# Kernel optimization log

Hardware: AMD Instinct MI355X
Metric: run time of the kernel (lower is better)

The kernel has to match this reference:

```python
import jax, jax.numpy as jnp
import numpy as np

B, C, D, H, W = 2, 512, 32, 32, 32
L, CTX = 256, 768
NH, HD, G = 8, 64, 8
EPS = 1e-5


def group_norm(x, w, b):
    Bb, Cc, Dd, Hh, Ww = x.shape
    xg = x.reshape(Bb, G, Cc // G, Dd, Hh, Ww)
    mu = xg.mean(axis=(2, 3, 4, 5), keepdims=True)
    var = xg.var(axis=(2, 3, 4, 5), keepdims=True)
    xn = ((xg - mu) * jax.lax.rsqrt(var + EPS)).reshape(Bb, Cc, Dd, Hh, Ww)
    return xn * w[None, :, None, None, None] + b[None, :, None, None, None]


def layer_norm(x, w, b):
    mu = x.mean(axis=-1, keepdims=True)
    var = x.var(axis=-1, keepdims=True)
    return (x - mu) * jax.lax.rsqrt(var + EPS) * w + b


def setup_inputs() -> dict:
    key = jax.random.key(0)
    ks = jax.random.split(key, 8)
    s = 0.02  # weight init scale
    return {
        "x": jax.random.normal(ks[0], (B, C, D, H, W), jnp.float32),
        "context": jax.random.normal(ks[1], (B, L, CTX), jnp.float32),
        "gn_w": jnp.ones((C,), jnp.float32),
        "gn_b": jnp.zeros((C,), jnp.float32),
        "ln_w": jnp.ones((CTX,), jnp.float32),
        "ln_b": jnp.zeros((CTX,), jnp.float32),
        "q_w": jax.random.normal(ks[2], (C, C), jnp.float32) * s,
        "q_b": jnp.zeros((C,), jnp.float32),
        "k_w": jax.random.normal(ks[3], (C, CTX), jnp.float32) * s,
        "k_b": jnp.zeros((C,), jnp.float32),
        "v_w": jax.random.normal(ks[4], (C, CTX), jnp.float32) * s,
        "v_b": jnp.zeros((C,), jnp.float32),
        "proj_w": jax.random.normal(ks[5], (C, C), jnp.float32) * s,
        "proj_b": jnp.zeros((C,), jnp.float32),
    }


def reference(x, context, gn_w, gn_b, ln_w, ln_b, q_w, q_b, k_w, k_b, v_w, v_b, proj_w, proj_b):
    Bb, Cc, Dd, Hh, Ww = x.shape
    S = Dd * Hh * Ww
    h = group_norm(x, gn_w, gn_b)
    ctx = layer_norm(context, ln_w, ln_b)
    # 1x1 Conv3d == per-voxel linear over channels
    q = jnp.einsum('oc,bcdhw->bodhw', q_w, h) + q_b[None, :, None, None, None]
    q = q.reshape(Bb, NH, HD, S)                                        # (b,h,e,s)
    k = (ctx @ k_w.T + k_b).reshape(Bb, L, NH, HD).transpose(0, 2, 1, 3)  # (b,h,l,e)
    v = (ctx @ v_w.T + v_b).reshape(Bb, L, NH, HD).transpose(0, 2, 1, 3)  # (b,h,l,e)
    scale = HD ** -0.5
    attn = jnp.einsum('bhes,bhle->bhsl', q, k) * scale                  # (b,h,S,L)
    attn = jax.nn.softmax(attn, axis=-1)
    out = jnp.einsum('bhsl,bhle->bhes', attn, v).reshape(Bb, Cc, Dd, Hh, Ww)
    out = jnp.einsum('oc,bcdhw->bodhw', proj_w, out) + proj_b[None, :, None, None, None]
    return out + x
```

## Files before the change

### kernel.cpp

```cpp
#include <hip/hip_runtime.h>

typedef unsigned short u16;
typedef unsigned int u32;
typedef __attribute__((ext_vector_type(4))) float f32x4;
typedef __attribute__((ext_vector_type(8))) short bf16x8;
typedef __attribute__((ext_vector_type(8))) u16 u16x8;
typedef __attribute__((ext_vector_type(4))) u16 u16x4;
typedef __attribute__((ext_vector_type(4))) u32 u32x4;

#define DEVI __device__ __forceinline__

constexpr int C_ = 512, S_ = 32768, L_ = 256, CTX_ = 768;

DEVI u16 f2b(float f) {
    union { float f; unsigned u; } x; x.f = f;
    unsigned r = x.u + 0x7fffu + ((x.u >> 16) & 1u);
    return (u16)(r >> 16);
}

DEVI f32x4 mfma16(bf16x8 a, bf16x8 b, f32x4 c) {
    return __builtin_amdgcn_mfma_f32_16x16x32_bf16(a, b, c, 0, 0, 0);
}

DEVI void gload16(const void* g, void* l) {
    __builtin_amdgcn_global_load_lds(
        (const __attribute__((address_space(1))) void*)g,
        (__attribute__((address_space(3))) void*)l, 16, 0, 0);
}

DEVI u32 cvtpk(float lo, float hi) {
    u32 d;
    asm("v_cvt_pk_bf16_f32 %0, %1, %2" : "=v"(d) : "v"(lo), "v"(hi));
    return d;
}
DEVI void pl32(u32& a, u32& b) {
    asm volatile("v_permlane32_swap_b32 %0, %1" : "+v"(a), "+v"(b));
}
DEVI void pl16(u32& a, u32& b) {
    asm volatile("v_permlane16_swap_b32 %0, %1" : "+v"(a), "+v"(b));
}

__global__ __launch_bounds__(256) void prep_small(
    const float* __restrict__ a0, const float* __restrict__ a1,
    const float* __restrict__ a2, const float* __restrict__ a3,
    u16* __restrict__ o0, u16* __restrict__ o1,
    u16* __restrict__ o2, u16* __restrict__ o3,
    const float* __restrict__ ctx, const float* __restrict__ lw,
    const float* __restrict__ lb, u16* __restrict__ cn)
{
    const int which = blockIdx.y, tid = threadIdx.x;
    if (which < 4) {
        const float* src = which == 0 ? a0 : which == 1 ? a1 : which == 2 ? a2 : a3;
        u16* dst = which == 0 ? o0 : which == 1 ? o1 : which == 2 ? o2 : o3;
        int n4 = (which == 1 || which == 2) ? (512 * 768 / 4) : (512 * 512 / 4);
        int i = blockIdx.x * 256 + tid;
        if (i < n4) {
            float4 v = ((const float4*)src)[i];
            u16x4 o; o[0] = f2b(v.x); o[1] = f2b(v.y); o[2] = f2b(v.z); o[3] = f2b(v.w);
            ((u16x4*)dst)[i] = o;
        }
        return;
    }
    const int row = blockIdx.x;
    const float* p = ctx + (size_t)row * CTX_;
    float v0 = p[tid], v1 = p[tid + 256], v2 = p[tid + 512];
    float s1 = v0 + v1 + v2, s2 = v0 * v0 + v1 * v1 + v2 * v2;
    for (int m = 1; m < 64; m <<= 1) { s1 += __shfl_xor(s1, m); s2 += __shfl_xor(s2, m); }
    __shared__ float a1s[4], a2s[4];
    int w = tid >> 6, lane = tid & 63;
    if (lane == 0) { a1s[w] = s1; a2s[w] = s2; }
    __syncthreads();
    s1 = a1s[0] + a1s[1] + a1s[2] + a1s[3];
    s2 = a2s[0] + a2s[1] + a2s[2] + a2s[3];
    const float invN = 1.0f / 768.0f;
    float mu = s1 * invN, rstd = rsqrtf(s2 * invN - mu * mu + 1e-5f);
    u16* o = cn + (size_t)row * CTX_;
    o[tid]       = f2b((v0 - mu) * rstd * lw[tid]       + lb[tid]);
    o[tid + 256] = f2b((v1 - mu) * rstd * lw[tid + 256] + lb[tid + 256]);
    o[tid + 512] = f2b((v2 - mu) * rstd * lw[tid + 512] + lb[tid + 512]);
}

__global__ __launch_bounds__(256) void gn_partial(const float* __restrict__ x,
                                                  float* __restrict__ part)
{
    const int bg = blockIdx.y, blk = blockIdx.x, tid = threadIdx.x;
    const int cs = blk >> 5, sblk = blk & 31;
    const float* base = x + (size_t)(bg * 64 + cs * 32) * S_
                          + (size_t)sblk * 1024 + tid * 4;
    float s1 = 0.f, s2 = 0.f;
    for (int c = 0; c < 32; ++c) {
        float4 v = *(const float4*)(base + (size_t)c * S_);
        s1 += v.x + v.y + v.z + v.w;
        s2 += v.x * v.x + v.y * v.y + v.z * v.z + v.w * v.w;
    }
    for (int m = 1; m < 64; m <<= 1) { s1 += __shfl_xor(s1, m); s2 += __shfl_xor(s2, m); }
    __shared__ float a1[4], a2[4];
    int w = tid >> 6, lane = tid & 63;
    if (lane == 0) { a1[w] = s1; a2[w] = s2; }
    __syncthreads();
    if (tid == 0) {
        part[(bg * 64 + blk) * 2 + 0] = a1[0] + a1[1] + a1[2] + a1[3];
        part[(bg * 64 + blk) * 2 + 1] = a2[0] + a2[1] + a2[2] + a2[3];
    }
}

__global__ __launch_bounds__(64) void gn_final_coef(
    const float* __restrict__ part, const float* __restrict__ gw,
    const float* __restrict__ gb, float* __restrict__ ca, float* __restrict__ cb)
{
    int bg = blockIdx.x, tid = threadIdx.x;
    float s1 = part[(bg * 64 + tid) * 2];
    float s2 = part[(bg * 64 + tid) * 2 + 1];
    for (int m = 1; m < 64; m <<= 1) { s1 += __shfl_xor(s1, m); s2 += __shfl_xor(s2, m); }
    const float invN = 1.0f / (64.0f * (float)S_);
    float mu = __shfl(s1, 0) * invN;
    float var = __shfl(s2, 0) * invN - mu * mu;
    float rs = rsqrtf(var + 1e-5f);
    int z = bg >> 3, c = (bg & 7) * 64 + tid;
    float a = rs * gw[c];
    ca[z * 512 + c] = a;
    cb[z * 512 + c] = gb[c] - mu * a;
}

template <int MODE, bool SWAP>
__global__ __launch_bounds__(256, 4) void gemm_nt(
    const u16* __restrict__ A, const u16* __restrict__ Bp,
    const float* __restrict__ bias, void* __restrict__ outp,
    const float* __restrict__ resid, int K, int ldo,
    size_t aStride, size_t bStride, size_t oStride, float scale,
    const u16* __restrict__ Bp2, const float* __restrict__ bias2,
    void* __restrict__ outp2)
{
    __shared__ __align__(16) u16 lA[2][4096];
    __shared__ __align__(16) u16 lB[2][4096];
    const int tid = threadIdx.x;
    const int w = tid >> 6, lane = tid & 63;
    const int g = lane >> 4, r = lane & 15;

    const int nx = gridDim.x, nxy = nx * gridDim.y;
    const int raw = blockIdx.x + nx * blockIdx.y;
    const int tile = (raw & 7) * (nxy >> 3) + (raw >> 3);
    const int bx = tile % nx, by = tile / nx;
    const int m0 = (SWAP ? by : bx) * 128, n0 = (SWAP ? bx : by) * 128;
    const int z = blockIdx.z;
    A += (size_t)z * aStride;
    const u16* Bsel = Bp;
    if constexpr (MODE == 3) { if (z) Bsel = Bp2; }
    Bsel += (size_t)z * bStride;

    const int l8 = lane & 7, lh = lane >> 3;
    const int u_ = l8 ^ lh;
    const int mro = (lh << 1) + (u_ >> 2);
    const int kco = (u_ & 3) * 8;
    const int wr = w >> 1, wc = w & 1;
    const int nt = K >> 5;

    f32x4 acc[4][4];
#pragma unroll
    for (int m = 0; m < 4; ++m)
#pragma unroll
        for (int n = 0; n < 4; ++n) acc[m][n] = f32x4{0.f, 0.f, 0.f, 0.f};

#define STAGE_B(t, bi_) {                                                      \
    size_t ko_ = (size_t)((t) * 32 + kco);                                     \
    _Pragma("unroll")                                                          \
    for (int j = 0; j < 2; ++j) {                                              \
        int grow_ = w * 32 + j * 16 + mro;                                     \
        gload16(Bsel + (size_t)(n0 + grow_) * K + ko_,                         \
                &lB[bi_][(w * 16 + j * 8) << 6]);                              \
    } }

#define STAGE_A(t, bi_) {                                                      \
    size_t ko_ = (size_t)((t) * 32 + kco);                                     \
    _Pragma("unroll")                                                          \
    for (int j = 0; j < 2; ++j) {                                              \
        int grow_ = w * 32 + j * 16 + mro;                                     \
        gload16(A + (size_t)(m0 + grow_) * K + ko_,                            \
                &lA[bi_][(w * 16 + j * 8) << 6]);                              \
    } }

    const float* xA = nullptr;
    const float* cAp = nullptr;
    const float* cBp = nullptr;
    int cp2 = 0, sb = 0, zc = 0;
    f32x4 a00{}, a01{}, a10{}, a11{};
    float2 ka{}, kb{};
    if constexpr (MODE == 4) {
        xA = resid + (size_t)z * ((size_t)C_ * S_);
        cAp = bias2;
        cBp = (const float*)outp2;
        cp2 = (tid >> 4) * 2;
        sb = (tid & 15) * 8;
        zc = z * 512;
    }

#define LOAD_A4(t) {                                                           \
    int c0n_ = (t) * 32 + cp2;                                                 \
    const float* r0_ = xA + (size_t)c0n_ * S_ + m0 + sb;                       \
    a00 = *(const f32x4*)r0_;  a01 = *(const f32x4*)(r0_ + 4);                 \
    a10 = *(const f32x4*)(r0_ + S_); a11 = *(const f32x4*)(r0_ + S_ + 4);      \
    ka = *(const float2*)&cAp[zc + c0n_];                                      \
    kb = *(const float2*)&cBp[zc + c0n_]; }

#define WRITE_A4(bi_) {                                                        \
    _Pragma("unroll")                                                          \
    for (int j = 0; j < 8; ++j) {                                              \
        float v0_ = ((j < 4) ? a00[j] : a01[j - 4]) * ka.x + kb.x;             \
        float v1_ = ((j < 4) ? a10[j] : a11[j - 4]) * ka.y + kb.y;             \
        int mm_ = sb + j;                                                      \
        int idx_ = ((mm_ >> 1) << 6)                                           \
            + (((((mm_ & 1) << 2) + (cp2 >> 3)) ^ ((mm_ >> 1) & 7)) << 3)      \
            + (cp2 & 7);                                                       \
        *(u32*)&lA[bi_][idx_] = cvtpk(v0_, v1_);                               \
    } }

    if constexpr (MODE == 4) {
        STAGE_B(0, 0);
        LOAD_A4(0);
        WRITE_A4(0);
        __syncthreads();
        for (int t = 0; t < nt; ++t) {
            const int cur = t & 1;
            if (t + 1 < nt) {
                STAGE_B(t + 1, cur ^ 1);
                LOAD_A4(t + 1);
            }
            bf16x8 af[4], bf_[4];
#pragma unroll
            for (int m = 0; m < 4; ++m) {
                int row = wr * 32 + m * 8 + (r >> 1);
                int slot = (((r & 1) << 2) + g) ^ ((r >> 1) & 7);
                af[m] = *(const bf16x8*)&lA[cur][(row << 6) + (slot << 3)];
            }
#pragma unroll
            for (int n = 0; n < 4; ++n) {
                int row = wc * 32 + n * 8 + (r >> 1);
                int slot = (((r & 1) << 2) + g) ^ ((r >> 1) & 7);
                bf_[n] = *(const bf16x8*)&lB[cur][(row << 6) + (slot << 3)];
            }
#pragma unroll
            for (int m = 0; m < 4; ++m)
#pragma unroll
                for (int n = 0; n < 4; ++n)
                    acc[m][n] = mfma16(bf_[n], af[m], acc[m][n]);
            if (t + 1 < nt) WRITE_A4(cur ^ 1);
            __syncthreads();
        }
    } else {
        STAGE_A(0, 0);
        STAGE_B(0, 0);
        for (int t = 0; t < nt; ++t) {
            const int cur = t & 1;
            if (t + 1 < nt) {
                STAGE_A(t + 1, cur ^ 1);
                STAGE_B(t + 1, cur ^ 1);
                asm volatile("s_waitcnt vmcnt(4)" ::: "memory");
            } else {
                asm volatile("s_waitcnt vmcnt(0)" ::: "memory");
            }
            __builtin_amdgcn_s_barrier();
            bf16x8 af[4], bf_[4];
#pragma unroll
            for (int m = 0; m < 4; ++m) {
                int row = wr * 32 + m * 8 + (r >> 1);
                int slot = (((r & 1) << 2) + g) ^ ((r >> 1) & 7);
                af[m] = *(const bf16x8*)&lA[cur][(row << 6) + (slot << 3)];
            }
#pragma unroll
            for (int n = 0; n < 4; ++n) {
                int row = wc * 32 + n * 8 + (r >> 1);
                int slot = (((r & 1) << 2) + g) ^ ((r >> 1) & 7);
                bf_[n] = *(const bf16x8*)&lB[cur][(row << 6) + (slot << 3)];
            }
#pragma unroll
            for (int m = 0; m < 4; ++m)
#pragma unroll
                for (int n = 0; n < 4; ++n)
                    acc[m][n] = mfma16(bf_[n], af[m], acc[m][n]);
            __builtin_amdgcn_s_barrier();
        }
    }
#undef STAGE_A
#undef STAGE_B
#undef LOAD_A4
#undef WRITE_A4

    if constexpr (MODE == 0 || MODE == 4) {
        u16* ob = (u16*)outp + (size_t)z * oStride;
#pragma unroll
        for (int m = 0; m < 4; ++m) {
            int gm = m0 + wr * 64 + m * 16 + r;
#pragma unroll
            for (int n = 0; n < 4; ++n) {
                int gn0 = n0 + wc * 64 + n * 16 + g * 4;
                float4 bn = *(const float4*)&bias[gn0];
                u32 w0 = cvtpk(acc[m][n][0] * scale + bn.x * scale,
                               acc[m][n][1] * scale + bn.y * scale);
                u32 w1 = cvtpk(acc[m][n][2] * scale + bn.z * scale,
                               acc[m][n][3] * scale + bn.w * scale);
                *(uint2*)&ob[(size_t)gm * ldo + gn0] = make_uint2(w0, w1);
            }
        }
    } else if constexpr (MODE == 2) {
        float* of = (float*)outp + (size_t)z * oStride;
        const float* rs = resid + (size_t)z * oStride;
#pragma unroll
        for (int m = 0; m < 4; ++m) {
            int gm = m0 + wr * 64 + m * 16 + r;
            float bm = bias[gm];
#pragma unroll
            for (int n = 0; n < 4; ++n) {
                int gn0 = n0 + wc * 64 + n * 16 + g * 4;
                size_t idx = (size_t)gm * ldo + gn0;
                float4 rv = *(const float4*)&rs[idx];
                float4 o4;
                o4.x = acc[m][n][0] + bm + rv.x;
                o4.y = acc[m][n][1] + bm + rv.y;
                o4.z = acc[m][n][2] + bm + rv.z;
                o4.w = acc[m][n][3] + bm + rv.w;
                *(float4*)&of[idx] = o4;
            }
        }
    } else if constexpr (MODE == 3) {
        if (z == 0) {
            u16* ob = (u16*)outp;
#pragma unroll
            for (int m = 0; m < 4; ++m) {
                int gm = m0 + wr * 64 + m * 16 + r;
#pragma unroll
                for (int n = 0; n < 4; ++n) {
                    int gn0 = n0 + wc * 64 + n * 16 + g * 4;
                    float4 bn = *(const float4*)&bias[gn0];
                    u32 w0 = cvtpk(acc[m][n][0] + bn.x, acc[m][n][1] + bn.y);
                    u32 w1 = cvtpk(acc[m][n][2] + bn.z, acc[m][n][3] + bn.w);
                    *(uint2*)&ob[(size_t)gm * ldo + gn0] = make_uint2(w0, w1);
                }
            }
        } else {
            u16* ob = (u16*)outp2;
#pragma unroll
            for (int m = 0; m < 4; ++m) {
                int gm = m0 + wr * 64 + m * 16 + r;
                int bb = gm >> 8, l = gm & 255;
#pragma unroll
                for (int n = 0; n < 4; ++n) {
                    int gn0 = n0 + wc * 64 + n * 16 + g * 4;
#pragma unroll
                    for (int i = 0; i < 4; ++i)
                        ob[((size_t)(bb * 512 + gn0 + i)) * 256 + l] =
                            f2b(acc[m][n][i] + bias2[gn0 + i]);
                }
            }
        }
    }
}

__global__ __launch_bounds__(256, 2) void attn_kernel(
    const u16* __restrict__ q, const u16* __restrict__ kk,
    const u16* __restrict__ vv, u16* __restrict__ ao)
{
    __shared__ __align__(16) u16 sm[32768];
    const int tid = threadIdx.x;
    const int w = tid >> 6, lane = tid & 63;
    const int g = lane >> 4, r = lane & 15;
    const int bh = blockIdx.y, b = bh >> 3, h = bh & 7;
    const int s0 = blockIdx.x * 128;

    {
        const u16* kbase = kk + ((size_t)b * L_) * C_ + h * 64;
#pragma unroll
        for (int j = 0; j < 8; ++j) {
            int idx = j * 256 + tid;
            int l = idx >> 3, ch = idx & 7;
            u16x8 val = *(const u16x8*)(kbase + (size_t)l * C_ + ch * 8);
            *(u16x8*)&sm[l * 64 + ((ch ^ (l & 7)) << 3)] = val;
        }
        const u16* vbase = vv + ((size_t)bh * 64) * 256;
#pragma unroll
        for (int j = 0; j < 8; ++j) {
            int idx = j * 256 + tid;
            int e = idx >> 5, ch = idx & 31;
            u16x8 val = *(const u16x8*)(vbase + (size_t)e * 256 + ch * 8);
            *(u16x8*)&sm[16384 + e * 256 + ((ch ^ (e & 7)) << 3)] = val;
        }
    }

    const int sw = s0 + w * 32;
    bf16x8 qf[2][2];
#pragma unroll
    for (int m = 0; m < 2; ++m)
#pragma unroll
        for (int kt = 0; kt < 2; ++kt)
            qf[m][kt] = *(const bf16x8*)(q + ((size_t)(b * S_ + sw + m * 16 + r)) * C_
                                         + h * 64 + kt * 32 + g * 8);
    __syncthreads();

    f32x4 accs[2][16];
#pragma unroll
    for (int m = 0; m < 2; ++m)
#pragma unroll
        for (int n = 0; n < 16; ++n) accs[m][n] = f32x4{0.f, 0.f, 0.f, 0.f};
    __builtin_amdgcn_s_setprio(1);
#pragma unroll
    for (int n = 0; n < 16; ++n) {
#pragma unroll
        for (int kt = 0; kt < 2; ++kt) {
            int c = kt * 4 + g;
            bf16x8 kf = *(const bf16x8*)&sm[(n * 16 + r) * 64 + ((c ^ (r & 7)) << 3)];
#pragma unroll
            for (int m = 0; m < 2; ++m) accs[m][n] = mfma16(kf, qf[m][kt], accs[m][n]);
        }
    }
    __builtin_amdgcn_s_setprio(0);

    float inv[2];
#pragma unroll
    for (int m = 0; m < 2; ++m) {
        float mx = accs[m][0][0];
#pragma unroll
        for (int n = 0; n < 16; ++n)
#pragma unroll
            for (int i = 0; i < 4; ++i) mx = fmaxf(mx, accs[m][n][i]);
        mx = fmaxf(mx, __shfl_xor(mx, 16));
        mx = fmaxf(mx, __shfl_xor(mx, 32));
        float sum = 0.f;
#pragma unroll
        for (int n = 0; n < 16; ++n)
#pragma unroll
            for (int i = 0; i < 4; ++i) {
                float e = __expf(accs[m][n][i] - mx);
                accs[m][n][i] = e; sum += e;
            }
        sum += __shfl_xor(sum, 16);
        sum += __shfl_xor(sum, 32);
        inv[m] = 1.0f / sum;
    }

    f32x4 acco[2][4];
#pragma unroll
    for (int m = 0; m < 2; ++m)
#pragma unroll
        for (int n = 0; n < 4; ++n) acco[m][n] = f32x4{0.f, 0.f, 0.f, 0.f};

#pragma unroll
    for (int c = 0; c < 8; ++c) {
        bf16x8 pa[2];
#pragma unroll
        for (int m = 0; m < 2; ++m) {
            u32 x0 = cvtpk(accs[m][2 * c][0] * inv[m], accs[m][2 * c][1] * inv[m]);
            u32 x1 = cvtpk(accs[m][2 * c][2] * inv[m], accs[m][2 * c][3] * inv[m]);
            u32 y0 = cvtpk(accs[m][2 * c + 1][0] * inv[m], accs[m][2 * c + 1][1] * inv[m]);
            u32 y1 = cvtpk(accs[m][2 * c + 1][2] * inv[m], accs[m][2 * c + 1][3] * inv[m]);
            pl32(x0, y0);
            pl32(x1, y1);
            pl16(x0, y0);
            pl16(x1, y1);
            u32x4 pw; pw[0] = x0; pw[1] = x1; pw[2] = y0; pw[3] = y1;
            pa[m] = *(bf16x8*)&pw;
        }
        bf16x8 vf[4];
#pragma unroll
        for (int n = 0; n < 4; ++n) {
            int e = n * 16 + r;
            vf[n] = *(const bf16x8*)&sm[16384 + e * 256 + (((c * 4 + g) ^ (r & 7)) << 3)];
        }
        __builtin_amdgcn_s_setprio(1);
#pragma unroll
        for (int m = 0; m < 2; ++m)
#pragma unroll
            for (int n = 0; n < 4; ++n)
                acco[m][n] = mfma16(vf[n], pa[m], acco[m][n]);
        __builtin_amdgcn_s_setprio(0);
    }

#pragma unroll
    for (int m = 0; m < 2; ++m) {
        const size_t rowb = ((size_t)(b * S_ + sw + m * 16 + r)) * C_ + h * 64;
#pragma unroll
        for (int n = 0; n < 4; ++n) {
            u32 w0 = cvtpk(acco[m][n][0], acco[m][n][1]);
            u32 w1 = cvtpk(acco[m][n][2], acco[m][n][3]);
            *(uint2*)&ao[rowb + n * 16 + g * 4] = make_uint2(w0, w1);
        }
    }
}

extern "C" void kernel_launch(void* const* d_in, const int* in_sizes, int n_in,
                              void* d_out, int out_size, void* d_ws, size_t ws_size,
                              hipStream_t stream)
{
    (void)in_sizes; (void)n_in; (void)out_size; (void)ws_size;
    const float* x    = (const float*)d_in[0];
    const float* ctx  = (const float*)d_in[1];
    const float* gn_w = (const float*)d_in[2];
    const float* gn_b = (const float*)d_in[3];
    const float* ln_w = (const float*)d_in[4];
    const float* ln_b = (const float*)d_in[5];
    const float* q_w  = (const float*)d_in[6];
    const float* q_b  = (const float*)d_in[7];
    const float* k_w  = (const float*)d_in[8];
    const float* k_b  = (const float*)d_in[9];
    const float* v_w  = (const float*)d_in[10];
    const float* v_b  = (const float*)d_in[11];
    const float* p_w  = (const float*)d_in[12];
    const float* p_b  = (const float*)d_in[13];
    float* out = (float*)d_out;

    char* ws = (char*)d_ws;
    constexpr size_t WS_WQ   = 0;
    constexpr size_t WS_WK   = WS_WQ + (size_t)512 * 512 * 2;
    constexpr size_t WS_WV   = WS_WK + (size_t)512 * 768 * 2;
    constexpr size_t WS_WP   = WS_WV + (size_t)512 * 768 * 2;
    constexpr size_t WS_PART = WS_WP + (size_t)512 * 512 * 2;
    constexpr size_t WS_CA   = WS_PART + (size_t)16 * 64 * 2 * 4;
    constexpr size_t WS_CB   = WS_CA + 4096;
    constexpr size_t WS_CTXN = WS_CB + 4096;
    constexpr size_t WS_K    = WS_CTXN + (size_t)512 * 768 * 2;
    constexpr size_t WS_V    = WS_K + (size_t)2 * 8 * 256 * 64 * 2;
    constexpr size_t WS_Q    = WS_V + (size_t)2 * 8 * 256 * 64 * 2;
    constexpr size_t WS_H    = WS_Q + (size_t)2 * 32768 * 512 * 2;

    u16* wq = (u16*)(ws + WS_WQ);
    u16* wk = (u16*)(ws + WS_WK);
    u16* wv = (u16*)(ws + WS_WV);
    u16* wp = (u16*)(ws + WS_WP);
    float* part  = (float*)(ws + WS_PART);
    float* coefA = (float*)(ws + WS_CA);
    float* coefB = (float*)(ws + WS_CB);
    u16* ctxn = (u16*)(ws + WS_CTXN);
    u16* kt   = (u16*)(ws + WS_K);
    u16* vt   = (u16*)(ws + WS_V);
    u16* qt   = (u16*)(ws + WS_Q);
    u16* ao   = (u16*)(ws + WS_H);

    const size_t bsc = (size_t)S_ * C_;

    gn_partial<<<dim3(64, 16), 256, 0, stream>>>(x, part);
    prep_small<<<dim3(512, 5), 256, 0, stream>>>(q_w, k_w, v_w, p_w,
                                                 wq, wk, wv, wp,
                                                 ctx, ln_w, ln_b, ctxn);
    gn_final_coef<<<16, 64, 0, stream>>>(part, gn_w, gn_b, coefA, coefB);
    gemm_nt<4, true><<<dim3(4, 256, 2), 256, 0, stream>>>(
        nullptr, wq, q_b, qt, x, 512, 512, 0, 0, bsc, 0.125f,
        nullptr, coefA, coefB);
    gemm_nt<3, false><<<dim3(4, 4, 2), 256, 0, stream>>>(
        ctxn, wk, k_b, kt, nullptr, 768, 512, 0, 0, 0, 1.0f,
        wv, v_b, vt);
    attn_kernel<<<dim3(256, 16), 256, 0, stream>>>(qt, kt, vt, ao);
    gemm_nt<2, false><<<dim3(4, 256, 2), 256, 0, stream>>>(
        wp, ao, p_b, out, x, 512, S_, 0, bsc, bsc, 1.0f,
        nullptr, nullptr, nullptr);
}
```

Baseline: 270.7 us.

## Fold GroupNorm affine into Q weights and feed bf16 x copy to Q GEMM

New measurement: 275.6 us. Within noise of the previous version (+1.8%).

```diff
diff --git a/kernel.cpp b/kernel.cpp
--- a/kernel.cpp
+++ b/kernel.cpp
@@ -81,17 +81,21 @@
 }
 
 __global__ __launch_bounds__(256) void gn_partial(const float* __restrict__ x,
-                                                  float* __restrict__ part)
+                                                  float* __restrict__ part,
+                                                  u16* __restrict__ xbf)
 {
     const int bg = blockIdx.y, blk = blockIdx.x, tid = threadIdx.x;
     const int cs = blk >> 5, sblk = blk & 31;
-    const float* base = x + (size_t)(bg * 64 + cs * 32) * S_
-                          + (size_t)sblk * 1024 + tid * 4;
+    const size_t cbase = (size_t)(bg * 64 + cs * 32);
+    const size_t soff = (size_t)sblk * 1024 + tid * 4;
+    const float* base = x + cbase * S_ + soff;
     float s1 = 0.f, s2 = 0.f;
     for (int c = 0; c < 32; ++c) {
         float4 v = *(const float4*)(base + (size_t)c * S_);
         s1 += v.x + v.y + v.z + v.w;
         s2 += v.x * v.x + v.y * v.y + v.z * v.z + v.w * v.w;
+        u16x4 o; o[0] = f2b(v.x); o[1] = f2b(v.y); o[2] = f2b(v.z); o[3] = f2b(v.w);
+        *(u16x4*)&xbf[(cbase + c) * S_ + soff] = o;
     }
     for (int m = 1; m < 64; m <<= 1) { s1 += __shfl_xor(s1, m); s2 += __shfl_xor(s2, m); }
     __shared__ float a1[4], a2[4];
@@ -122,6 +126,39 @@
     cb[z * 512 + c] = gb[c] - mu * a;
 }
 
+__global__ __launch_bounds__(256) void fold_w(
+    const float* __restrict__ qw, const float* __restrict__ qb,
+    const float* __restrict__ ca, const float* __restrict__ cb,
+    u16* __restrict__ wq2, float* __restrict__ qb2)
+{
+    const int z = blockIdx.y, tid = threadIdx.x;
+    const int o0 = blockIdx.x * 32;
+    {
+        int ow = tid >> 3, seg = tid & 7;
+        int o = o0 + ow;
+        const float* wrow = qw + (size_t)o * 512;
+        const float* cbz = cb + z * 512;
+        float s = 0.f;
+        for (int c = seg * 64; c < seg * 64 + 64; ++c) s += wrow[c] * cbz[c];
+        s += __shfl_xor(s, 1); s += __shfl_xor(s, 2); s += __shfl_xor(s, 4);
+        if (seg == 0) qb2[z * 512 + o] = qb[o] + s;
+    }
+    {
+        const float* caz = ca + z * 512;
+        size_t base = (size_t)z * 512 * 512 + (size_t)o0 * 512;
+        int e0 = tid * 64;
+        for (int j = 0; j < 64; j += 4) {
+            int e = e0 + j;
+            int orow = o0 + (e >> 9), c = e & 511;
+            u16x4 pk;
+#pragma unroll
+            for (int i = 0; i < 4; ++i)
+                pk[i] = f2b(qw[(size_t)orow * 512 + c + i] * caz[c + i]);
+            *(u16x4*)&wq2[base + e] = pk;
+        }
+    }
+}
+
 template <int MODE, bool SWAP>
 __global__ __launch_bounds__(256, 4) void gemm_nt(
     const u16* __restrict__ A, const u16* __restrict__ Bp,
@@ -179,51 +216,40 @@
                 &lA[bi_][(w * 16 + j * 8) << 6]);                              \
     } }
 
-    const float* xA = nullptr;
-    const float* cAp = nullptr;
-    const float* cBp = nullptr;
-    int cp2 = 0, sb = 0, zc = 0;
-    f32x4 a00{}, a01{}, a10{}, a11{};
-    float2 ka{}, kb{};
-    if constexpr (MODE == 4) {
-        xA = resid + (size_t)z * ((size_t)C_ * S_);
-        cAp = bias2;
-        cBp = (const float*)outp2;
+    int cp2 = 0, sb = 0;
+    u16x8 ax0{}, ax1{};
+    if constexpr (MODE == 5) {
         cp2 = (tid >> 4) * 2;
         sb = (tid & 15) * 8;
-        zc = z * 512;
-    }
-
-#define LOAD_A4(t) {                                                           \
+    }
+
+#define LOAD_A5(t) {                                                           \
     int c0n_ = (t) * 32 + cp2;                                                 \
-    const float* r0_ = xA + (size_t)c0n_ * S_ + m0 + sb;                       \
-    a00 = *(const f32x4*)r0_;  a01 = *(const f32x4*)(r0_ + 4);                 \
-    a10 = *(const f32x4*)(r0_ + S_); a11 = *(const f32x4*)(r0_ + S_ + 4);      \
-    ka = *(const float2*)&cAp[zc + c0n_];                                      \
-    kb = *(const float2*)&cBp[zc + c0n_]; }
-
-#define WRITE_A4(bi_) {                                                        \
+    const u16* r0_ = A + (size_t)c0n_ * S_ + m0 + sb;                          \
+    ax0 = *(const u16x8*)r0_;                                                  \
+    ax1 = *(const u16x8*)(r0_ + S_); }
+
+#define WRITE_A5(bi_) {                                                        \
     _Pragma("unroll")                                                          \
     for (int j = 0; j < 8; ++j) {                                              \
-        float v0_ = ((j < 4) ? a00[j] : a01[j - 4]) * ka.x + kb.x;             \
-        float v1_ = ((j < 4) ? a10[j] : a11[j - 4]) * ka.y + kb.y;             \
+        u32 wrd_ = (u32)ax0[j] | ((u32)ax1[j] << 16);                          \
         int mm_ = sb + j;                                                      \
         int idx_ = ((mm_ >> 1) << 6)                                           \
             + (((((mm_ & 1) << 2) + (cp2 >> 3)) ^ ((mm_ >> 1) & 7)) << 3)      \
             + (cp2 & 7);                                                       \
-        *(u32*)&lA[bi_][idx_] = cvtpk(v0_, v1_);                               \
+        *(u32*)&lA[bi_][idx_] = wrd_;                                          \
     } }
 
-    if constexpr (MODE == 4) {
+    if constexpr (MODE == 5) {
         STAGE_B(0, 0);
-        LOAD_A4(0);
-        WRITE_A4(0);
+        LOAD_A5(0);
+        WRITE_A5(0);
         __syncthreads();
         for (int t = 0; t < nt; ++t) {
             const int cur = t & 1;
             if (t + 1 < nt) {
                 STAGE_B(t + 1, cur ^ 1);
-                LOAD_A4(t + 1);
+                LOAD_A5(t + 1);
             }
             bf16x8 af[4], bf_[4];
 #pragma unroll
@@ -243,7 +269,7 @@
 #pragma unroll
                 for (int n = 0; n < 4; ++n)
                     acc[m][n] = mfma16(bf_[n], af[m], acc[m][n]);
-            if (t + 1 < nt) WRITE_A4(cur ^ 1);
+            if (t + 1 < nt) WRITE_A5(cur ^ 1);
             __syncthreads();
         }
     } else {
@@ -282,10 +308,10 @@
     }
 #undef STAGE_A
 #undef STAGE_B
-#undef LOAD_A4
-#undef WRITE_A4
-
-    if constexpr (MODE == 0 || MODE == 4) {
+#undef LOAD_A5
+#undef WRITE_A5
+
+    if constexpr (MODE == 0 || MODE == 5) {
         u16* ob = (u16*)outp + (size_t)z * oStride;
 #pragma unroll
         for (int m = 0; m < 4; ++m) {
@@ -293,7 +319,8 @@
 #pragma unroll
             for (int n = 0; n < 4; ++n) {
                 int gn0 = n0 + wc * 64 + n * 16 + g * 4;
-                float4 bn = *(const float4*)&bias[gn0];
+                const float* bp = (MODE == 5) ? &bias[z * 512 + gn0] : &bias[gn0];
+                float4 bn = *(const float4*)bp;
                 u32 w0 = cvtpk(acc[m][n][0] * scale + bn.x * scale,
                                acc[m][n][1] * scale + bn.y * scale);
                 u32 w1 = cvtpk(acc[m][n][2] * scale + bn.z * scale,
@@ -514,7 +541,9 @@
     constexpr size_t WS_PART = WS_WP + (size_t)512 * 512 * 2;
     constexpr size_t WS_CA   = WS_PART + (size_t)16 * 64 * 2 * 4;
     constexpr size_t WS_CB   = WS_CA + 4096;
-    constexpr size_t WS_CTXN = WS_CB + 4096;
+    constexpr size_t WS_WQ2  = WS_CB + 4096;
+    constexpr size_t WS_QB2  = WS_WQ2 + (size_t)2 * 512 * 512 * 2;
+    constexpr size_t WS_CTXN = WS_QB2 + 4096;
     constexpr size_t WS_K    = WS_CTXN + (size_t)512 * 768 * 2;
     constexpr size_t WS_V    = WS_K + (size_t)2 * 8 * 256 * 64 * 2;
     constexpr size_t WS_Q    = WS_V + (size_t)2 * 8 * 256 * 64 * 2;
@@ -527,22 +556,26 @@
     float* part  = (float*)(ws + WS_PART);
     float* coefA = (float*)(ws + WS_CA);
     float* coefB = (float*)(ws + WS_CB);
+    u16* wq2  = (u16*)(ws + WS_WQ2);
+    float* qb2 = (float*)(ws + WS_QB2);
     u16* ctxn = (u16*)(ws + WS_CTXN);
     u16* kt   = (u16*)(ws + WS_K);
     u16* vt   = (u16*)(ws + WS_V);
     u16* qt   = (u16*)(ws + WS_Q);
     u16* ao   = (u16*)(ws + WS_H);
+    u16* xbf  = ao;
 
     const size_t bsc = (size_t)S_ * C_;
 
-    gn_partial<<<dim3(64, 16), 256, 0, stream>>>(x, part);
+    gn_partial<<<dim3(64, 16), 256, 0, stream>>>(x, part, xbf);
     prep_small<<<dim3(512, 5), 256, 0, stream>>>(q_w, k_w, v_w, p_w,
                                                  wq, wk, wv, wp,
                                                  ctx, ln_w, ln_b, ctxn);
     gn_final_coef<<<16, 64, 0, stream>>>(part, gn_w, gn_b, coefA, coefB);
-    gemm_nt<4, true><<<dim3(4, 256, 2), 256, 0, stream>>>(
-        nullptr, wq, q_b, qt, x, 512, 512, 0, 0, bsc, 0.125f,
-        nullptr, coefA, coefB);
+    fold_w<<<dim3(16, 2), 256, 0, stream>>>(q_w, q_b, coefA, coefB, wq2, qb2);
+    gemm_nt<5, true><<<dim3(4, 256, 2), 256, 0, stream>>>(
+        xbf, wq2, qb2, qt, nullptr, 512, 512, bsc, (size_t)512 * 512, bsc,
+        0.125f, nullptr, nullptr, nullptr);
     gemm_nt<3, false><<<dim3(4, 4, 2), 256, 0, stream>>>(
         ctxn, wk, k_b, kt, nullptr, 768, 512, 0, 0, 0, 1.0f,
         wv, v_b, vt);
```
